# Kernel optimization log

Hardware: AMD Instinct MI355X
Metric: run time of the kernel (lower is better)

Reference implementation:

```python
import jax, jax.numpy as jnp
import numpy as np

N_WORDS = 8192   # total words across all concepts
L = 24           # chars per word (padded)
D = 256          # word_vec_d
H = 8            # attention heads
DFF = 1024
VOCAB = 128
N_CONCEPTS = 1024
MAXW = 16        # max_words
GROUPS = 4       # n_names: 4 equal groups of concepts


def setup_inputs() -> dict:
    key = jax.random.key(0)
    ks = jax.random.split(key, 9)
    rng = np.random.default_rng(0)
    # char tokens in [1, VOCAB), ragged word lengths in [4, L], tail = 0 (pad)
    vals = rng.integers(1, VOCAB, size=(N_WORDS, L))
    lens = rng.integers(4, L + 1, size=(N_WORDS,))
    inputs = np.where(np.arange(L)[None, :] < lens[:, None], vals, 0)
    # ragged words-per-concept: alternate 4 / 12 -> sums to N_WORDS, <= MAXW
    counts = np.where(np.arange(N_CONCEPTS) % 2 == 0, 4, 12)
    concept_id = np.repeat(np.arange(N_CONCEPTS), counts)
    word_pos = np.concatenate([np.arange(c) for c in counts])

    def w(k, shape):
        return 0.02 * jax.random.normal(k, shape, jnp.float32)

    return {
        "inputs": jnp.asarray(inputs, jnp.int32),
        "concept_id": jnp.asarray(concept_id, jnp.int32),
        "word_pos": jnp.asarray(word_pos, jnp.int32),
        "n_concepts": N_CONCEPTS,
        "n_names": GROUPS,
        "we_emb": w(ks[0], (VOCAB, D)),
        "we_qkv": w(ks[1], (D, 3 * D)),
        "we_o": w(ks[2], (D, D)),
        "we_ff1": w(ks[3], (D, DFF)),
        "we_ff2": w(ks[4], (DFF, D)),
        "ne_qkv": w(ks[5], (D, 3 * D)),
        "ne_o": w(ks[6], (D, D)),
        "ne_ff1": w(ks[7], (D, DFF)),
        "ne_ff2": w(ks[8], (DFF, D)),
    }


def _ln(x):
    m = x.mean(-1, keepdims=True)
    v = ((x - m) ** 2).mean(-1, keepdims=True)
    return (x - m) * jax.lax.rsqrt(v + 1e-5)


def _mha(x, wqkv, wo, key_pad=None):
    n, l, d = x.shape
    hd = d // H
    q, k, v = jnp.split(x @ wqkv, 3, axis=-1)
    q = q.reshape(n, l, H, hd)
    k = k.reshape(n, l, H, hd)
    v = v.reshape(n, l, H, hd)
    s = jnp.einsum('nqhd,nkhd->nhqk', q, k) / jnp.sqrt(jnp.asarray(hd, x.dtype))
    if key_pad is not None:
        s = jnp.where(key_pad[:, None, None, :], -1e9, s)
    a = jax.nn.softmax(s, axis=-1)
    o = jnp.einsum('nhqk,nkhd->nqhd', a, v).reshape(n, l, d)
    return o @ wo


def _block(x, wqkv, wo, w1, w2, key_pad=None):
    h = _ln(x + _mha(x, wqkv, wo, key_pad))
    return _ln(h + jax.nn.relu(h @ w1) @ w2)


def reference(inputs, concept_id, word_pos, n_concepts, n_names,
              we_emb, we_qkv, we_o, we_ff1, we_ff2,
              ne_qkv, ne_o, ne_ff1, ne_ff2):
    pad_mask = inputs == 0  # [N_WORDS, L]
    x = we_emb[inputs]      # [N_WORDS, L, D]
    word_ft = _block(x, we_qkv, we_o, we_ff1, we_ff2, pad_mask)
    # masked mean over chars -> one vector per word
    np_mask = (~pad_mask)[..., None].astype(word_ft.dtype)  # [N_WORDS, L, 1]
    name_vec = (word_ft * np_mask).sum(1) / np_mask.sum(1)   # [N_WORDS, D]
    # ragged -> padded: one scatter instead of per-sample torch.cat
    padded = jnp.zeros((n_concepts, MAXW, name_vec.shape[-1]), name_vec.dtype)
    padded = padded.at[concept_id, word_pos].set(name_vec)   # [n_concepts, MAXW, D]
    name_ft = _block(padded, ne_qkv, ne_o, ne_ff1, ne_ff2)
    row_pad = (padded == 0).all(-1, keepdims=True)           # all-zero rows = pad words
    name_ft = jnp.where(row_pad, jnp.zeros((), name_ft.dtype), name_ft)
    counts = (name_ft != 0).sum(1).astype(name_ft.dtype)     # [n_concepts, D]
    pooled = name_ft.sum(1) / counts                         # [n_concepts, D]
    return tuple(jnp.split(pooled, n_names, axis=0))
```

## Files before the change

kernel.cpp:

```cpp
#include <hip/hip_runtime.h>
#include <hip/hip_bf16.h>

#define NWORDS 8192
#define LW 24
#define DIM 256
#define NHEAD 8
#define DFF 1024
#define NCONC 1024
#define MAXW 16
#define TN (NCONC * MAXW)

typedef float floatx4 __attribute__((ext_vector_type(4)));
typedef short shortx8 __attribute__((ext_vector_type(8)));

__device__ __forceinline__ float bf2f(ushort u) {
  union { uint u; float f; } v; v.u = ((uint)u) << 16; return v.f;
}
__device__ __forceinline__ ushort f2bf(float f) {
  __hip_bfloat16 h = __float2bfloat16(f);
  return *reinterpret_cast<ushort*>(&h);
}

__device__ __forceinline__ void load_lds16(const ushort* gsrc, ushort* lds) {
  __builtin_amdgcn_global_load_lds((const __attribute__((address_space(1))) void*)gsrc,
                                   (__attribute__((address_space(3))) void*)lds, 16, 0, 0);
}

#define WAIT_VM0() __builtin_amdgcn_s_waitcnt(0x0F70)
#define WAIT_LGKM0() __builtin_amdgcn_s_waitcnt(0xC07F)

#define STAGE_COL(lane) ((((lane) & 3) ^ (((lane) >> 3) & 3)) * 8)
#define FRAG_OFF(row, quad) (((row) * 32) + ((((quad) ^ (((row) >> 1) & 3))) * 8))

struct WPSeg { const float* W; ushort* WT; int K; int N; int b0; };
struct WPAll { WPSeg seg[8]; };

__global__ __launch_bounds__(256) void wprep_all(WPAll a, int nseg) {
  int b = blockIdx.x;
  int s = 0;
#pragma unroll
  for (int i = 1; i < 8; i++)
    if (i < nseg && b >= a.seg[i].b0) s = i;
  const WPSeg sg = a.seg[s];
  int idx = (b - sg.b0) * 256 + threadIdx.x;
  if (idx < sg.K * sg.N) {
    int k = idx / sg.N, n = idx % sg.N;
    sg.WT[n * sg.K + k] = f2bf(sg.W[idx]);
  }
}

__global__ __launch_bounds__(256) void embed8(const int* __restrict__ inputs,
                                              const float* __restrict__ we_emb,
                                              ushort* __restrict__ x, int ntok) {
  int idx = blockIdx.x * 256 + threadIdx.x;
  int t = idx >> 5, d = (idx & 31) * 8;
  if (t < ntok) {
    const float4* src = (const float4*)&we_emb[inputs[t] * DIM + d];
    const float4 f0 = src[0], f1 = src[1];
    uint4 o;
    o.x = (uint)f2bf(f0.x) | ((uint)f2bf(f0.y) << 16);
    o.y = (uint)f2bf(f0.z) | ((uint)f2bf(f0.w) << 16);
    o.z = (uint)f2bf(f1.x) | ((uint)f2bf(f1.y) << 16);
    o.w = (uint)f2bf(f1.z) | ((uint)f2bf(f1.w) << 16);
    *(uint4*)&x[(size_t)t * DIM + d] = o;
  }
}

template <bool LN, int NTILES>
__global__ __launch_bounds__(256, 2) void gemm_tok64(const ushort* __restrict__ A, int lda,
                                                     const ushort* __restrict__ BT,
                                                     const ushort* __restrict__ RES,
                                                     ushort* __restrict__ C, int ldc) {
  __shared__ __align__(16) ushort As[8 * 64 * 32];
  __shared__ __align__(16) ushort Wb[256 * 32];
  __shared__ float red1[64 * 4];
  __shared__ float red2[64 * 4];
  const int tid = threadIdx.x;
  const int w = tid >> 6, lane = tid & 63;
  const int quad = lane >> 4, l16 = lane & 15;
  const long m0 = (long)blockIdx.y * 64;
  const long nb0 = (long)blockIdx.x * NTILES * 256;
  const int srow = lane >> 2;
  const int scol = STAGE_COL(lane);
  const int wc = w * 64;

#pragma unroll
  for (int t = 0; t < 8; t++) {
    int p = 2 * w + t / 4, ii = t % 4;
    load_lds16(&A[(m0 + ii * 16 + srow) * lda + p * 32 + scol], &As[p * 2048 + (ii * 16) * 32]);
  }
#pragma unroll
  for (int ii = 0; ii < 4; ii++)
    load_lds16(&BT[(nb0 + wc + ii * 16 + srow) * 256 + scol], &Wb[(wc + ii * 16) * 32]);
  __syncthreads();

#pragma unroll 1
  for (int nt = 0; nt < NTILES; nt++) {
    const long nb = nb0 + (long)nt * 256;
    floatx4 acc[4][4] = {};
#pragma unroll 1
    for (int p = 0; p < 8; p++) {
      WAIT_VM0();
      shortx8 a[4], b[4];
#pragma unroll
      for (int j = 0; j < 4; j++)
        b[j] = *(const shortx8*)&Wb[FRAG_OFF(wc + j * 16 + l16, quad)];
      WAIT_LGKM0();
      if (p < 7) {
#pragma unroll
        for (int ii = 0; ii < 4; ii++)
          load_lds16(&BT[(nb + wc + ii * 16 + srow) * 256 + (p + 1) * 32 + scol],
                     &Wb[(wc + ii * 16) * 32]);
      } else if (nt < NTILES - 1) {
#pragma unroll
        for (int ii = 0; ii < 4; ii++)
          load_lds16(&BT[(nb + 256 + wc + ii * 16 + srow) * 256 + scol],
                     &Wb[(wc + ii * 16) * 32]);
      }
#pragma unroll
      for (int i = 0; i < 4; i++)
        a[i] = *(const shortx8*)&As[p * 2048 + FRAG_OFF(i * 16 + l16, quad)];
#pragma unroll
      for (int i = 0; i < 4; i++)
#pragma unroll
        for (int j = 0; j < 4; j++)
          acc[i][j] = __builtin_amdgcn_mfma_f32_16x16x32_bf16(a[i], b[j], acc[i][j], 0, 0, 0);
    }

    if (!LN) {
#pragma unroll
      for (int i = 0; i < 4; i++)
#pragma unroll
        for (int j = 0; j < 4; j++)
#pragma unroll
          for (int r = 0; r < 4; r++) {
            long m = m0 + i * 16 + quad * 4 + r;
            C[m * ldc + nb + wc + j * 16 + l16] = f2bf(acc[i][j][r]);
          }
    } else {
#pragma unroll
      for (int i = 0; i < 4; i++)
#pragma unroll
        for (int r = 0; r < 4; r++) {
          int row = i * 16 + quad * 4 + r;
          float s1 = 0.f, s2 = 0.f;
#pragma unroll
          for (int j = 0; j < 4; j++) {
            float v = acc[i][j][r] + bf2f(RES[(m0 + row) * 256 + wc + j * 16 + l16]);
            acc[i][j][r] = v;
            s1 += v;
            s2 += v * v;
          }
#pragma unroll
          for (int off = 1; off < 16; off <<= 1) {
            s1 += __shfl_xor(s1, off);
            s2 += __shfl_xor(s2, off);
          }
          if (l16 == 0) { red1[row * 4 + w] = s1; red2[row * 4 + w] = s2; }
        }
      __syncthreads();
#pragma unroll
      for (int i = 0; i < 4; i++)
#pragma unroll
        for (int r = 0; r < 4; r++) {
          int row = i * 16 + quad * 4 + r;
          float s1 = red1[row * 4] + red1[row * 4 + 1] + red1[row * 4 + 2] + red1[row * 4 + 3];
          float s2 = red2[row * 4] + red2[row * 4 + 1] + red2[row * 4 + 2] + red2[row * 4 + 3];
          float mean = s1 * (1.f / 256.f);
          float rstd = rsqrtf(s2 * (1.f / 256.f) - mean * mean + 1e-5f);
#pragma unroll
          for (int j = 0; j < 4; j++)
            C[(m0 + row) * 256 + wc + j * 16 + l16] = f2bf((acc[i][j][r] - mean) * rstd);
        }
    }
  }
}

__global__ __launch_bounds__(256, 2) void ffn_fused(const ushort* __restrict__ H,
                                                    const ushort* __restrict__ W1T,
                                                    const ushort* __restrict__ W2T,
                                                    ushort* __restrict__ C,
                                                    int M) {
  __shared__ __align__(16) ushort As[8 * 64 * 32];
  __shared__ __align__(16) ushort Ss[8 * 64 * 32];
  __shared__ __align__(16) ushort Wb[256 * 32];
  const int tid = threadIdx.x;
  const int w = tid >> 6, lane = tid & 63;
  const int quad = lane >> 4, l16 = lane & 15;
  const long m0 = (long)blockIdx.x * 64;
  const int srow = lane >> 2;
  const int scol = STAGE_COL(lane);

#pragma unroll
  for (int t = 0; t < 8; t++) {
    int p = 2 * w + t / 4, ii = t % 4;
    load_lds16(&H[(m0 + ii * 16 + srow) * 256 + p * 32 + scol], &As[(p * 2048) + (ii * 16) * 32]);
  }
#pragma unroll
  for (int ii = 0; ii < 4; ii++)
    load_lds16(&W1T[(long)(w * 64 + ii * 16 + srow) * 256 + scol], &Wb[(w * 64 + ii * 16) * 32]);
  __syncthreads();

  floatx4 acc2[4][4] = {};
  for (int m = 0; m < 4; m++) {
    floatx4 acc1[4][4] = {};
    if (m > 0) {
#pragma unroll
      for (int ii = 0; ii < 4; ii++)
        load_lds16(&W1T[(long)(m * 256 + w * 64 + ii * 16 + srow) * 256 + scol],
                   &Wb[(w * 64 + ii * 16) * 32]);
    }
#pragma unroll 1
    for (int p = 0; p < 8; p++) {
      WAIT_VM0();
      shortx8 a[4], b[4];
#pragma unroll
      for (int i = 0; i < 4; i++)
        a[i] = *(const shortx8*)&Wb[FRAG_OFF(w * 64 + i * 16 + l16, quad)];
      WAIT_LGKM0();
      if (p < 7) {
#pragma unroll
        for (int ii = 0; ii < 4; ii++)
          load_lds16(&W1T[(long)(m * 256 + w * 64 + ii * 16 + srow) * 256 + (p + 1) * 32 + scol],
                     &Wb[(w * 64 + ii * 16) * 32]);
      }
#pragma unroll
      for (int j = 0; j < 4; j++)
        b[j] = *(const shortx8*)&As[p * 2048 + FRAG_OFF(j * 16 + l16, quad)];
#pragma unroll
      for (int i = 0; i < 4; i++)
#pragma unroll
        for (int j = 0; j < 4; j++)
          acc1[i][j] = __builtin_amdgcn_mfma_f32_16x16x32_bf16(a[i], b[j], acc1[i][j], 0, 0, 0);
    }
    __syncthreads();
#pragma unroll
    for (int i = 0; i < 4; i++) {
      int fb = w * 64 + i * 16 + quad * 4;
      int pf = fb >> 5, c = (fb >> 3) & 3, off = fb & 7;
#pragma unroll
      for (int j = 0; j < 4; j++) {
        int tok = j * 16 + l16;
        ushort4 pk;
        pk.x = f2bf(fmaxf(acc1[i][j][0], 0.f));
        pk.y = f2bf(fmaxf(acc1[i][j][1], 0.f));
        pk.z = f2bf(fmaxf(acc1[i][j][2], 0.f));
        pk.w = f2bf(fmaxf(acc1[i][j][3], 0.f));
        *(ushort4*)&Ss[(pf * 64 + tok) * 32 + ((c ^ ((tok >> 1) & 3)) << 3) + off] = pk;
      }
    }
    __syncthreads();
#pragma unroll
    for (int jj = 0; jj < 4; jj++)
      load_lds16(&W2T[(long)(w * 64 + jj * 16 + srow) * 1024 + m * 256 + scol],
                 &Wb[(w * 64 + jj * 16) * 32]);
#pragma unroll 1
    for (int p = 0; p < 8; p++) {
      WAIT_VM0();
      shortx8 a[4], b[4];
#pragma unroll
      for (int j = 0; j < 4; j++)
        b[j] = *(const shortx8*)&Wb[FRAG_OFF(w * 64 + j * 16 + l16, quad)];
      WAIT_LGKM0();
      if (p < 7) {
#pragma unroll
        for (int jj = 0; jj < 4; jj++)
          load_lds16(&W2T[(long)(w * 64 + jj * 16 + srow) * 1024 + m * 256 + (p + 1) * 32 + scol],
                     &Wb[(w * 64 + jj * 16) * 32]);
      }
#pragma unroll
      for (int i = 0; i < 4; i++)
        a[i] = *(const shortx8*)&Ss[p * 2048 + FRAG_OFF(i * 16 + l16, quad)];
#pragma unroll
      for (int i = 0; i < 4; i++)
#pragma unroll
        for (int j = 0; j < 4; j++)
          acc2[i][j] = __builtin_amdgcn_mfma_f32_16x16x32_bf16(a[i], b[j], acc2[i][j], 0, 0, 0);
    }
  }
  __syncthreads();

  float* red1 = (float*)Ss;
  float* red2 = red1 + 256;
  const int wc = w * 64;
#pragma unroll
  for (int i = 0; i < 4; i++)
#pragma unroll
    for (int r = 0; r < 4; r++) {
      int row = i * 16 + quad * 4 + r;
      float s1 = 0.f, s2 = 0.f;
#pragma unroll
      for (int j = 0; j < 4; j++) {
        float v = acc2[i][j][r] + bf2f(H[(m0 + row) * 256 + wc + j * 16 + l16]);
        acc2[i][j][r] = v;
        s1 += v;
        s2 += v * v;
      }
#pragma unroll
      for (int off = 1; off < 16; off <<= 1) {
        s1 += __shfl_xor(s1, off);
        s2 += __shfl_xor(s2, off);
      }
      if (l16 == 0) { red1[row * 4 + w] = s1; red2[row * 4 + w] = s2; }
    }
  __syncthreads();
#pragma unroll
  for (int i = 0; i < 4; i++)
#pragma unroll
    for (int r = 0; r < 4; r++) {
      int row = i * 16 + quad * 4 + r;
      float s1 = red1[row * 4] + red1[row * 4 + 1] + red1[row * 4 + 2] + red1[row * 4 + 3];
      float s2 = red2[row * 4] + red2[row * 4 + 1] + red2[row * 4 + 2] + red2[row * 4 + 3];
      float mean = s1 * (1.f / 256.f);
      float rstd = rsqrtf(s2 * (1.f / 256.f) - mean * mean + 1e-5f);
      if (m0 + row < M) {
#pragma unroll
        for (int j = 0; j < 4; j++)
          C[(m0 + row) * 256 + wc + j * 16 + l16] = f2bf((acc2[i][j][r] - mean) * rstd);
      }
    }
}

template <int LSEQ, bool MASKED>
__global__ __launch_bounds__(256) void attn(const int* __restrict__ inputs,
                                            ushort* __restrict__ qkv) {
  __shared__ __align__(16) ushort Qs[32 * 256];
  __shared__ __align__(16) ushort Ks[32 * 256];
  __shared__ __align__(16) ushort Vt[256 * 32];
  __shared__ __align__(16) ushort Ps[4 * 32 * 32];
  __shared__ float pads[32];
  constexpr int MT = (LSEQ + 15) / 16;
  const int blk = blockIdx.x;
  const int tid = threadIdx.x;
  const int w = tid >> 6, lane = tid & 63;
  const int quad = lane >> 4, l16 = lane & 15;
  ushort* base = qkv + (size_t)blk * LSEQ * 768;
  const uint4* src = (const uint4*)base;
  const uint4 z4 = {0u, 0u, 0u, 0u};

  for (int i = tid; i < (32 - LSEQ) * 32 * 2; i += 256) {
    int arr = (i >= (32 - LSEQ) * 32);
    int rem = arr ? i - (32 - LSEQ) * 32 : i;
    int row = LSEQ + (rem >> 5), ch = rem & 31;
    *(uint4*)&((arr ? Ks : Qs)[row * 256 + ch * 8]) = z4;
  }
  for (int i = tid; i < 256 * (4 - LSEQ / 8); i += 256) {
    int row = i & 255, pc = LSEQ / 8 + (i >> 8);
    *(uint4*)&Vt[row * 32 + ((pc ^ ((row >> 3) & 3)) * 8)] = z4;
  }
  {
    ushort* pz = Ps + w * 1024;
    *(uint4*)&pz[lane * 16] = z4;
    *(uint4*)&pz[lane * 16 + 8] = z4;
  }
  if (tid < 32) {
    float pv = 1.f;
    if (tid < LSEQ) pv = MASKED ? ((inputs[blk * LSEQ + tid] == 0) ? 1.f : 0.f) : 0.f;
    pads[tid] = pv;
  }
  for (int i = tid; i < LSEQ * 96; i += 256) {
    int c = i / 96, part = i % 96;
    uint4 val = src[c * 96 + part];
    int sect = part >> 5, off = part & 31;
    if (sect == 0) {
      *(uint4*)&Qs[c * 256 + ((off ^ (c & 7)) * 8)] = val;
    } else if (sect == 1) {
      *(uint4*)&Ks[c * 256 + ((off ^ (c & 7)) * 8)] = val;
    } else {
      int d0 = (off & 31) * 8;
      const ushort* us = (const ushort*)&val;
#pragma unroll
      for (int j = 0; j < 8; j++) {
        int dim = d0 + j;
        Vt[dim * 32 + (((c >> 3) ^ ((dim >> 3) & 3)) * 8) + (c & 7)] = us[j];
      }
    }
  }
  __syncthreads();

  ushort* Psw = Ps + w * 1024;
#pragma unroll
  for (int t = 0; t < 2; t++) {
    const int h = w * 2 + t, hb = h * 32;
    shortx8 aq[MT], bk[MT];
#pragma unroll
    for (int i = 0; i < MT; i++)
      aq[i] = *(const shortx8*)&Qs[(i * 16 + l16) * 256 + (((h * 4 + quad) ^ (l16 & 7)) * 8)];
#pragma unroll
    for (int j = 0; j < MT; j++)
      bk[j] = *(const shortx8*)&Ks[(j * 16 + l16) * 256 + (((h * 4 + quad) ^ (l16 & 7)) * 8)];
    floatx4 s[MT][MT];
#pragma unroll
    for (int i = 0; i < MT; i++)
#pragma unroll
      for (int j = 0; j < MT; j++) {
        floatx4 zz = {0.f, 0.f, 0.f, 0.f};
        s[i][j] = __builtin_amdgcn_mfma_f32_16x16x32_bf16(aq[i], bk[j], zz, 0, 0, 0);
      }
    float pv[MT];
#pragma unroll
    for (int j = 0; j < MT; j++) pv[j] = pads[j * 16 + l16];
#pragma unroll
    for (int i = 0; i < MT; i++) {
#pragma unroll
      for (int r = 0; r < 4; r++) {
        float v[MT];
        float mx = -3e38f;
#pragma unroll
        for (int j = 0; j < MT; j++) {
          float x = s[i][j][r] * 0.17677669529663687f;
          if (pv[j] != 0.f) x = -1e9f;
          v[j] = x;
          mx = fmaxf(mx, x);
        }
#pragma unroll
        for (int off = 1; off < 16; off <<= 1) mx = fmaxf(mx, __shfl_xor(mx, off));
        float den = 0.f;
#pragma unroll
        for (int j = 0; j < MT; j++) { v[j] = __expf(v[j] - mx); den += v[j]; }
#pragma unroll
        for (int off = 1; off < 16; off <<= 1) den += __shfl_xor(den, off);
        float inv = 1.f / den;
        int row = i * 16 + quad * 4 + r;
#pragma unroll
        for (int j = 0; j < MT; j++) {
          int col = j * 16 + l16;
          Psw[row * 32 + (((col >> 3) ^ ((row >> 1) & 3)) * 8) + (col & 7)] = f2bf(v[j] * inv);
        }
      }
    }
    WAIT_LGKM0();
    shortx8 pa[MT], bv[2];
#pragma unroll
    for (int i = 0; i < MT; i++) {
      int row = i * 16 + l16;
      pa[i] = *(const shortx8*)&Psw[row * 32 + ((quad ^ ((row >> 1) & 3)) * 8)];
    }
#pragma unroll
    for (int jj = 0; jj < 2; jj++) {
      int row = hb + jj * 16 + l16;
      bv[jj] = *(const shortx8*)&Vt[row * 32 + ((quad ^ ((row >> 3) & 3)) * 8)];
    }
    floatx4 o[MT][2];
#pragma unroll
    for (int i = 0; i < MT; i++)
#pragma unroll
      for (int jj = 0; jj < 2; jj++) {
        floatx4 zz = {0.f, 0.f, 0.f, 0.f};
        o[i][jj] = __builtin_amdgcn_mfma_f32_16x16x32_bf16(pa[i], bv[jj], zz, 0, 0, 0);
      }
#pragma unroll
    for (int i = 0; i < MT; i++)
#pragma unroll
      for (int r = 0; r < 4; r++) {
        int row = i * 16 + quad * 4 + r;
        if (row < LSEQ) {
#pragma unroll
          for (int jj = 0; jj < 2; jj++)
            base[(size_t)row * 768 + hb + jj * 16 + l16] = f2bf(o[i][jj][r]);
        }
      }
  }
}

__global__ __launch_bounds__(256) void pool_scatter(const ushort* __restrict__ ft,
                                                    const int* __restrict__ inputs,
                                                    const int* __restrict__ cid,
                                                    const int* __restrict__ wpos,
                                                    ushort* __restrict__ padded,
                                                    int* __restrict__ flags) {
  int w = blockIdx.x, d = threadIdx.x;
  float s = 0.f;
  int cnt = 0;
  for (int c = 0; c < LW; c++) {
    if (inputs[w * LW + c] != 0) {
      s += bf2f(ft[((size_t)w * LW + c) * DIM + d]);
      cnt++;
    }
  }
  int slot = cid[w] * MAXW + wpos[w];
  padded[(size_t)slot * DIM + d] = f2bf(s / (float)cnt);
  if (d == 0) flags[slot] = 1;
}

__global__ __launch_bounds__(256) void final_pool(const ushort* __restrict__ nft,
                                                  const int* __restrict__ flags,
                                                  float* __restrict__ out) {
  int n = blockIdx.x, d = threadIdx.x;
  float s = 0.f;
  int cnt = 0;
  for (int wd = 0; wd < MAXW; wd++) {
    if (flags[n * MAXW + wd]) {
      s += bf2f(nft[((size_t)n * MAXW + wd) * DIM + d]);
      cnt++;
    }
  }
  out[n * DIM + d] = s / (float)cnt;
}

extern "C" void kernel_launch(void* const* d_in, const int* in_sizes, int n_in,
                              void* d_out, int out_size, void* d_ws, size_t ws_size,
                              hipStream_t stream) {
  const int* inputs = (const int*)d_in[0];
  const int* cid = (const int*)d_in[1];
  const int* wpos = (const int*)d_in[2];
  const float* we_emb = (const float*)d_in[5];
  const float* we_qkv = (const float*)d_in[6];
  const float* we_o = (const float*)d_in[7];
  const float* we_ff1 = (const float*)d_in[8];
  const float* we_ff2 = (const float*)d_in[9];
  const float* ne_qkv = (const float*)d_in[10];
  const float* ne_o = (const float*)d_in[11];
  const float* ne_ff1 = (const float*)d_in[12];
  const float* ne_ff2 = (const float*)d_in[13];
  float* out = (float*)d_out;

  int chunks = 4;
  if (ws_size >= 515000000UL) chunks = 1;
  else if (ws_size >= 263258112UL) chunks = 2;
  const int wpc = NWORDS / chunks;
  const int tpc = wpc * LW;

  const size_t X = (size_t)tpc * DIM * 2;
  const size_t Q = (size_t)tpc * 768 * 2;

  char* base = (char*)d_ws;
  ushort* x = (ushort*)(base);
  ushort* qkv = (ushort*)(base + X);
  ushort* h = (ushort*)(base + X + Q);
  ushort* ft = qkv;
  size_t pend = X + Q + X;
  ushort* padded = (ushort*)(base + pend);
  int* flags = (int*)(base + pend + 8388608);
  ushort* wT = (ushort*)(base + pend + 8454144);
  ushort* nqkv = (ushort*)(base);
  ushort* nh = (ushort*)(base + 25165824);
  ushort* nft = (ushort*)(base + 33554432);

  ushort* wqkvT = wT;
  ushort* woT = wT + 196608;
  ushort* wff1T = wT + 262144;
  ushort* wff2T = wT + 524288;
  ushort* nqkvT = wT + 786432;
  ushort* neoT = wT + 983040;
  ushort* neff1T = wT + 1048576;
  ushort* neff2T = wT + 1310720;

  {
    WPAll a;
    a.seg[0] = {we_qkv, wqkvT, 256, 768, 0};
    a.seg[1] = {we_o, woT, 256, 256, 768};
    a.seg[2] = {we_ff1, wff1T, 256, 1024, 1024};
    a.seg[3] = {we_ff2, wff2T, 1024, 256, 2048};
    a.seg[4] = {ne_qkv, nqkvT, 256, 768, 3072};
    a.seg[5] = {ne_o, neoT, 256, 256, 3840};
    a.seg[6] = {ne_ff1, neff1T, 256, 1024, 4096};
    a.seg[7] = {ne_ff2, neff2T, 1024, 256, 5120};
    wprep_all<<<6144, 256, 0, stream>>>(a, 8);
  }

  (void)hipMemsetAsync(padded, 0, (size_t)TN * DIM * 2, stream);
  (void)hipMemsetAsync(flags, 0, TN * 4, stream);

  for (int c = 0; c < chunks; c++) {
    const int* in_c = inputs + (size_t)c * wpc * LW;
    const int* cid_c = cid + (size_t)c * wpc;
    const int* wpos_c = wpos + (size_t)c * wpc;

    embed8<<<tpc / 8, 256, 0, stream>>>(in_c, we_emb, x, tpc);
    {
      dim3 g(1, tpc / 64);
      gemm_tok64<false, 3><<<g, 256, 0, stream>>>(x, 256, wqkvT, nullptr, qkv, 768);
    }
    attn<24, true><<<wpc, 256, 0, stream>>>(in_c, qkv);
    {
      dim3 g(1, tpc / 64);
      gemm_tok64<true, 1><<<g, 256, 0, stream>>>(qkv, 768, woT, x, h, 256);
    }
    ffn_fused<<<tpc / 64, 256, 0, stream>>>(h, wff1T, wff2T, ft, tpc);
    pool_scatter<<<wpc, 256, 0, stream>>>(ft, in_c, cid_c, wpos_c, padded, flags);
  }

  {
    dim3 g(1, TN / 64);
    gemm_tok64<false, 3><<<g, 256, 0, stream>>>(padded, 256, nqkvT, nullptr, nqkv, 768);
  }
  attn<16, false><<<NCONC, 256, 0, stream>>>(nullptr, nqkv);
  {
    dim3 g(1, TN / 64);
    gemm_tok64<true, 1><<<g, 256, 0, stream>>>(nqkv, 768, neoT, padded, nh, 256);
  }
  ffn_fused<<<TN / 64, 256, 0, stream>>>(nh, neff1T, neff2T, nft, TN);
  final_pool<<<NCONC, 256, 0, stream>>>(nft, flags, out);
}
```

Measured before the change: 888.8 us.

## Fuse word-level QKV projection with attention in a single kernel

Adds a kernel that computes the QKV projection for two words (48 tokens) per block, keeps Q, K and transposed V in swizzled shared memory, and runs masked softmax attention there with MFMA. Only the attention output goes to global memory. This removes the round trip of the 768-wide QKV tensor through HBM and one kernel launch. In exchange the block uses a large amount of LDS at one block per SM, and its 48-row tiles leave some MFMA work on padded rows, so occupancy and tile efficiency may drop.

```diff
diff --git a/kernel.cpp b/kernel.cpp
--- a/kernel.cpp
+++ b/kernel.cpp
@@ -176,6 +176,187 @@
   }
 }
 
+__global__ __launch_bounds__(256, 1) void qkv_attn_fused(
+    const ushort* __restrict__ A,
+    const ushort* __restrict__ BT,
+    const int* __restrict__ inputs,
+    ushort* __restrict__ O) {
+  constexpr int LSEQ = 24, WPB = 2, ROWS = WPB * LSEQ;
+  __shared__ __align__(16) ushort As[8 * ROWS * 32];
+  __shared__ __align__(16) ushort Wb[256 * 32];
+  __shared__ __align__(16) ushort Qs[WPB][24 * 256];
+  __shared__ __align__(16) ushort Ks[WPB][24 * 256];
+  __shared__ __align__(16) ushort Vt[WPB][256 * 32];
+  __shared__ __align__(16) ushort Ps[4][32 * 32];
+  __shared__ float pads[WPB][32];
+  const int tid = threadIdx.x;
+  const int w = tid >> 6, lane = tid & 63;
+  const int quad = lane >> 4, l16 = lane & 15;
+  const int blk = blockIdx.x;
+  const long m0 = (long)blk * ROWS;
+  const int srow = lane >> 2;
+  const int scol = STAGE_COL(lane);
+  const int wc = w * 64;
+
+  if (tid < WPB * 32) {
+    int wd = tid >> 5, r = tid & 31;
+    pads[wd][r] = (r >= LSEQ || inputs[(blk * WPB + wd) * LW + r] == 0) ? 1.f : 0.f;
+  }
+#pragma unroll
+  for (int t = 0; t < 6; t++) {
+    int idx = w * 6 + t, p = idx / 3, ii = idx % 3;
+    load_lds16(&A[(m0 + ii * 16 + srow) * 256 + p * 32 + scol],
+               &As[p * (ROWS * 32) + (ii * 16) * 32]);
+  }
+#pragma unroll
+  for (int ii = 0; ii < 4; ii++)
+    load_lds16(&BT[(wc + ii * 16 + srow) * 256 + scol], &Wb[(wc + ii * 16) * 32]);
+  __syncthreads();
+
+#pragma unroll 1
+  for (int nt = 0; nt < 3; nt++) {
+    const long nb = (long)nt * 256;
+    floatx4 acc[3][4] = {};
+#pragma unroll 1
+    for (int p = 0; p < 8; p++) {
+      WAIT_VM0();
+      shortx8 a[3], b[4];
+#pragma unroll
+      for (int j = 0; j < 4; j++)
+        b[j] = *(const shortx8*)&Wb[FRAG_OFF(wc + j * 16 + l16, quad)];
+      WAIT_LGKM0();
+      if (p < 7) {
+#pragma unroll
+        for (int ii = 0; ii < 4; ii++)
+          load_lds16(&BT[(nb + wc + ii * 16 + srow) * 256 + (p + 1) * 32 + scol],
+                     &Wb[(wc + ii * 16) * 32]);
+      } else if (nt < 2) {
+#pragma unroll
+        for (int ii = 0; ii < 4; ii++)
+          load_lds16(&BT[(nb + 256 + wc + ii * 16 + srow) * 256 + scol],
+                     &Wb[(wc + ii * 16) * 32]);
+      }
+#pragma unroll
+      for (int i = 0; i < 3; i++)
+        a[i] = *(const shortx8*)&As[p * (ROWS * 32) + FRAG_OFF(i * 16 + l16, quad)];
+#pragma unroll
+      for (int i = 0; i < 3; i++)
+#pragma unroll
+        for (int j = 0; j < 4; j++)
+          acc[i][j] = __builtin_amdgcn_mfma_f32_16x16x32_bf16(a[i], b[j], acc[i][j], 0, 0, 0);
+    }
+#pragma unroll
+    for (int i = 0; i < 3; i++)
+#pragma unroll
+      for (int r = 0; r < 4; r++) {
+        int row = i * 16 + quad * 4 + r;
+        int wd = (row >= LSEQ) ? 1 : 0;
+        int tok = row - wd * LSEQ;
+#pragma unroll
+        for (int j = 0; j < 4; j++) {
+          int dim = wc + j * 16 + l16;
+          ushort val = f2bf(acc[i][j][r]);
+          if (nt == 0) {
+            Qs[wd][tok * 256 + (((dim >> 3) ^ (tok & 7)) << 3) + (dim & 7)] = val;
+          } else if (nt == 1) {
+            Ks[wd][tok * 256 + (((dim >> 3) ^ (tok & 7)) << 3) + (dim & 7)] = val;
+          } else {
+            Vt[wd][dim * 32 + ((((tok >> 3) ^ ((dim >> 3) & 3))) << 3) + (tok & 7)] = val;
+          }
+        }
+      }
+  }
+  __syncthreads();
+
+  const int wd = w >> 1;
+  ushort* Psw = Ps[w];
+  const ushort* Qw = Qs[wd];
+  const ushort* Kw = Ks[wd];
+  const ushort* Vw = Vt[wd];
+#pragma unroll 1
+  for (int t = 0; t < 4; t++) {
+    const int h = (w & 1) * 4 + t, hb = h * 32;
+    shortx8 aq[2], bk[2];
+#pragma unroll
+    for (int i = 0; i < 2; i++)
+      aq[i] = *(const shortx8*)&Qw[(i * 16 + l16) * 256 + (((h * 4 + quad) ^ (l16 & 7)) * 8)];
+#pragma unroll
+    for (int j = 0; j < 2; j++)
+      bk[j] = *(const shortx8*)&Kw[(j * 16 + l16) * 256 + (((h * 4 + quad) ^ (l16 & 7)) * 8)];
+    floatx4 s[2][2];
+#pragma unroll
+    for (int i = 0; i < 2; i++)
+#pragma unroll
+      for (int j = 0; j < 2; j++) {
+        floatx4 zz = {0.f, 0.f, 0.f, 0.f};
+        s[i][j] = __builtin_amdgcn_mfma_f32_16x16x32_bf16(aq[i], bk[j], zz, 0, 0, 0);
+      }
+    float pv[2];
+#pragma unroll
+    for (int j = 0; j < 2; j++) pv[j] = pads[wd][j * 16 + l16];
+#pragma unroll
+    for (int i = 0; i < 2; i++) {
+#pragma unroll
+      for (int r = 0; r < 4; r++) {
+        float v[2];
+        float mx = -3e38f;
+#pragma unroll
+        for (int j = 0; j < 2; j++) {
+          float x = s[i][j][r] * 0.17677669529663687f;
+          if (pv[j] != 0.f) x = -1e9f;
+          v[j] = x;
+          mx = fmaxf(mx, x);
+        }
+#pragma unroll
+        for (int off = 1; off < 16; off <<= 1) mx = fmaxf(mx, __shfl_xor(mx, off));
+        float den = 0.f;
+#pragma unroll
+        for (int j = 0; j < 2; j++) { v[j] = __expf(v[j] - mx); den += v[j]; }
+#pragma unroll
+        for (int off = 1; off < 16; off <<= 1) den += __shfl_xor(den, off);
+        float inv = 1.f / den;
+        int row = i * 16 + quad * 4 + r;
+#pragma unroll
+        for (int j = 0; j < 2; j++) {
+          int col = j * 16 + l16;
+          Psw[row * 32 + (((col >> 3) ^ ((row >> 1) & 3)) * 8) + (col & 7)] = f2bf(v[j] * inv);
+        }
+      }
+    }
+    WAIT_LGKM0();
+    shortx8 pa[2], bv[2];
+#pragma unroll
+    for (int i = 0; i < 2; i++) {
+      int row = i * 16 + l16;
+      pa[i] = *(const shortx8*)&Psw[row * 32 + ((quad ^ ((row >> 1) & 3)) * 8)];
+    }
+#pragma unroll
+    for (int jj = 0; jj < 2; jj++) {
+      int row = hb + jj * 16 + l16;
+      bv[jj] = *(const shortx8*)&Vw[row * 32 + ((quad ^ ((row >> 3) & 3)) * 8)];
+    }
+    floatx4 o[2][2];
+#pragma unroll
+    for (int i = 0; i < 2; i++)
+#pragma unroll
+      for (int jj = 0; jj < 2; jj++) {
+        floatx4 zz = {0.f, 0.f, 0.f, 0.f};
+        o[i][jj] = __builtin_amdgcn_mfma_f32_16x16x32_bf16(pa[i], bv[jj], zz, 0, 0, 0);
+      }
+#pragma unroll
+    for (int i = 0; i < 2; i++)
+#pragma unroll
+      for (int r = 0; r < 4; r++) {
+        int row = i * 16 + quad * 4 + r;
+        if (row < LSEQ) {
+#pragma unroll
+          for (int jj = 0; jj < 2; jj++)
+            O[(m0 + wd * LSEQ + row) * 256 + hb + jj * 16 + l16] = f2bf(o[i][jj][r]);
+        }
+      }
+  }
+}
+
 __global__ __launch_bounds__(256, 2) void ffn_fused(const ushort* __restrict__ H,
                                                     const ushort* __restrict__ W1T,
                                                     const ushort* __restrict__ W2T,
@@ -526,9 +707,9 @@
 
   char* base = (char*)d_ws;
   ushort* x = (ushort*)(base);
-  ushort* qkv = (ushort*)(base + X);
+  ushort* obuf = (ushort*)(base + X);
   ushort* h = (ushort*)(base + X + Q);
-  ushort* ft = qkv;
+  ushort* ft = obuf;
   size_t pend = X + Q + X;
   ushort* padded = (ushort*)(base + pend);
   int* flags = (int*)(base + pend + 8388608);
@@ -568,14 +749,10 @@
     const int* wpos_c = wpos + (size_t)c * wpc;
 
     embed8<<<tpc / 8, 256, 0, stream>>>(in_c, we_emb, x, tpc);
+    qkv_attn_fused<<<tpc / 48, 256, 0, stream>>>(x, wqkvT, in_c, obuf);
     {
       dim3 g(1, tpc / 64);
-      gemm_tok64<false, 3><<<g, 256, 0, stream>>>(x, 256, wqkvT, nullptr, qkv, 768);
-    }
-    attn<24, true><<<wpc, 256, 0, stream>>>(in_c, qkv);
-    {
-      dim3 g(1, tpc / 64);
-      gemm_tok64<true, 1><<<g, 256, 0, stream>>>(qkv, 768, woT, x, h, 256);
+      gemm_tok64<true, 1><<<g, 256, 0, stream>>>(obuf, 256, woT, x, h, 256);
     }
     ffn_fused<<<tpc / 64, 256, 0, stream>>>(h, wff1T, wff2T, ft, tpc);
     pool_scatter<<<wpc, 256, 0, stream>>>(ft, in_c, cid_c, wpos_c, padded, flags);
```

Result: slower. 978.1 us (+10.0%).

## Fuse attention output projection and LayerNorm into the FFN kernel

Applied to the files above, without the earlier changes.

Merges the separate Wo projection GEMM (with residual add and LayerNorm) into the FFN kernel. Each 64-token block computes the projection from the attention output, normalizes it into shared memory, and runs the FFN on it directly. This removes one kernel launch per stage and the write and re-read of the intermediate h buffer, and the FFN residual now comes from LDS. In exchange the fused kernel does more serial work per block and uses more registers, which may lower occupancy.

```diff
diff --git a/kernel.cpp b/kernel.cpp
--- a/kernel.cpp
+++ b/kernel.cpp
@@ -176,11 +176,14 @@
   }
 }
 
-__global__ __launch_bounds__(256, 2) void ffn_fused(const ushort* __restrict__ H,
-                                                    const ushort* __restrict__ W1T,
-                                                    const ushort* __restrict__ W2T,
-                                                    ushort* __restrict__ C,
-                                                    int M) {
+__global__ __launch_bounds__(256, 2) void oproj_ffn_fused(
+    const ushort* __restrict__ QKV,
+    const ushort* __restrict__ XR,
+    const ushort* __restrict__ WoT,
+    const ushort* __restrict__ W1T,
+    const ushort* __restrict__ W2T,
+    ushort* __restrict__ C,
+    int M) {
   __shared__ __align__(16) ushort As[8 * 64 * 32];
   __shared__ __align__(16) ushort Ss[8 * 64 * 32];
   __shared__ __align__(16) ushort Wb[256 * 32];
@@ -190,15 +193,89 @@
   const long m0 = (long)blockIdx.x * 64;
   const int srow = lane >> 2;
   const int scol = STAGE_COL(lane);
+  const int wc = w * 64;
 
 #pragma unroll
   for (int t = 0; t < 8; t++) {
     int p = 2 * w + t / 4, ii = t % 4;
-    load_lds16(&H[(m0 + ii * 16 + srow) * 256 + p * 32 + scol], &As[(p * 2048) + (ii * 16) * 32]);
+    load_lds16(&QKV[(m0 + ii * 16 + srow) * 768 + p * 32 + scol], &Ss[p * 2048 + (ii * 16) * 32]);
   }
 #pragma unroll
   for (int ii = 0; ii < 4; ii++)
-    load_lds16(&W1T[(long)(w * 64 + ii * 16 + srow) * 256 + scol], &Wb[(w * 64 + ii * 16) * 32]);
+    load_lds16(&WoT[(long)(wc + ii * 16 + srow) * 256 + scol], &Wb[(wc + ii * 16) * 32]);
+  __syncthreads();
+
+  floatx4 aco[4][4] = {};
+#pragma unroll 1
+  for (int p = 0; p < 8; p++) {
+    WAIT_VM0();
+    shortx8 a[4], b[4];
+#pragma unroll
+    for (int j = 0; j < 4; j++)
+      b[j] = *(const shortx8*)&Wb[FRAG_OFF(wc + j * 16 + l16, quad)];
+    WAIT_LGKM0();
+    if (p < 7) {
+#pragma unroll
+      for (int ii = 0; ii < 4; ii++)
+        load_lds16(&WoT[(long)(wc + ii * 16 + srow) * 256 + (p + 1) * 32 + scol],
+                   &Wb[(wc + ii * 16) * 32]);
+    }
+#pragma unroll
+    for (int i = 0; i < 4; i++)
+      a[i] = *(const shortx8*)&Ss[p * 2048 + FRAG_OFF(i * 16 + l16, quad)];
+#pragma unroll
+    for (int i = 0; i < 4; i++)
+#pragma unroll
+      for (int j = 0; j < 4; j++)
+        aco[i][j] = __builtin_amdgcn_mfma_f32_16x16x32_bf16(a[i], b[j], aco[i][j], 0, 0, 0);
+  }
+  __syncthreads();
+
+  {
+    float* red1 = (float*)Ss;
+    float* red2 = red1 + 256;
+#pragma unroll
+    for (int i = 0; i < 4; i++)
+#pragma unroll
+      for (int r = 0; r < 4; r++) {
+        int row = i * 16 + quad * 4 + r;
+        float s1 = 0.f, s2 = 0.f;
+#pragma unroll
+        for (int j = 0; j < 4; j++) {
+          float v = aco[i][j][r] + bf2f(XR[(m0 + row) * 256 + wc + j * 16 + l16]);
+          aco[i][j][r] = v;
+          s1 += v;
+          s2 += v * v;
+        }
+#pragma unroll
+        for (int off = 1; off < 16; off <<= 1) {
+          s1 += __shfl_xor(s1, off);
+          s2 += __shfl_xor(s2, off);
+        }
+        if (l16 == 0) { red1[row * 4 + w] = s1; red2[row * 4 + w] = s2; }
+      }
+    __syncthreads();
+#pragma unroll
+    for (int i = 0; i < 4; i++)
+#pragma unroll
+      for (int r = 0; r < 4; r++) {
+        int row = i * 16 + quad * 4 + r;
+        float s1 = red1[row * 4] + red1[row * 4 + 1] + red1[row * 4 + 2] + red1[row * 4 + 3];
+        float s2 = red2[row * 4] + red2[row * 4 + 1] + red2[row * 4 + 2] + red2[row * 4 + 3];
+        float mean = s1 * (1.f / 256.f);
+        float rstd = rsqrtf(s2 * (1.f / 256.f) - mean * mean + 1e-5f);
+#pragma unroll
+        for (int j = 0; j < 4; j++) {
+          int col = wc + j * 16 + l16;
+          int p = col >> 5, c = (col >> 3) & 3, off = col & 7;
+          As[p * 2048 + row * 32 + ((c ^ ((row >> 1) & 3)) << 3) + off] =
+              f2bf((aco[i][j][r] - mean) * rstd);
+        }
+      }
+  }
+#pragma unroll
+  for (int ii = 0; ii < 4; ii++)
+    load_lds16(&W1T[(long)(wc + ii * 16 + srow) * 256 + scol], &Wb[(wc + ii * 16) * 32]);
   __syncthreads();
 
   floatx4 acc2[4][4] = {};
@@ -207,8 +284,8 @@
     if (m > 0) {
 #pragma unroll
       for (int ii = 0; ii < 4; ii++)
-        load_lds16(&W1T[(long)(m * 256 + w * 64 + ii * 16 + srow) * 256 + scol],
-                   &Wb[(w * 64 + ii * 16) * 32]);
+        load_lds16(&W1T[(long)(m * 256 + wc + ii * 16 + srow) * 256 + scol],
+                   &Wb[(wc + ii * 16) * 32]);
     }
 #pragma unroll 1
     for (int p = 0; p < 8; p++) {
@@ -216,13 +293,13 @@
       shortx8 a[4], b[4];
 #pragma unroll
       for (int i = 0; i < 4; i++)
-        a[i] = *(const shortx8*)&Wb[FRAG_OFF(w * 64 + i * 16 + l16, quad)];
+        a[i] = *(const shortx8*)&Wb[FRAG_OFF(wc + i * 16 + l16, quad)];
       WAIT_LGKM0();
       if (p < 7) {
 #pragma unroll
         for (int ii = 0; ii < 4; ii++)
-          load_lds16(&W1T[(long)(m * 256 + w * 64 + ii * 16 + srow) * 256 + (p + 1) * 32 + scol],
-                     &Wb[(w * 64 + ii * 16) * 32]);
+          load_lds16(&W1T[(long)(m * 256 + wc + ii * 16 + srow) * 256 + (p + 1) * 32 + scol],
+                     &Wb[(wc + ii * 16) * 32]);
       }
 #pragma unroll
       for (int j = 0; j < 4; j++)
@@ -236,7 +313,7 @@
     __syncthreads();
 #pragma unroll
     for (int i = 0; i < 4; i++) {
-      int fb = w * 64 + i * 16 + quad * 4;
+      int fb = wc + i * 16 + quad * 4;
       int pf = fb >> 5, c = (fb >> 3) & 3, off = fb & 7;
 #pragma unroll
       for (int j = 0; j < 4; j++) {
@@ -252,21 +329,21 @@
     __syncthreads();
 #pragma unroll
     for (int jj = 0; jj < 4; jj++)
-      load_lds16(&W2T[(long)(w * 64 + jj * 16 + srow) * 1024 + m * 256 + scol],
-                 &Wb[(w * 64 + jj * 16) * 32]);
+      load_lds16(&W2T[(long)(wc + jj * 16 + srow) * 1024 + m * 256 + scol],
+                 &Wb[(wc + jj * 16) * 32]);
 #pragma unroll 1
     for (int p = 0; p < 8; p++) {
       WAIT_VM0();
       shortx8 a[4], b[4];
 #pragma unroll
       for (int j = 0; j < 4; j++)
-        b[j] = *(const shortx8*)&Wb[FRAG_OFF(w * 64 + j * 16 + l16, quad)];
+        b[j] = *(const shortx8*)&Wb[FRAG_OFF(wc + j * 16 + l16, quad)];
       WAIT_LGKM0();
       if (p < 7) {
 #pragma unroll
         for (int jj = 0; jj < 4; jj++)
-          load_lds16(&W2T[(long)(w * 64 + jj * 16 + srow) * 1024 + m * 256 + (p + 1) * 32 + scol],
-                     &Wb[(w * 64 + jj * 16) * 32]);
+          load_lds16(&W2T[(long)(wc + jj * 16 + srow) * 1024 + m * 256 + (p + 1) * 32 + scol],
+                     &Wb[(wc + jj * 16) * 32]);
       }
 #pragma unroll
       for (int i = 0; i < 4; i++)
@@ -282,7 +359,6 @@
 
   float* red1 = (float*)Ss;
   float* red2 = red1 + 256;
-  const int wc = w * 64;
 #pragma unroll
   for (int i = 0; i < 4; i++)
 #pragma unroll
@@ -291,7 +367,10 @@
       float s1 = 0.f, s2 = 0.f;
 #pragma unroll
       for (int j = 0; j < 4; j++) {
-        float v = acc2[i][j][r] + bf2f(H[(m0 + row) * 256 + wc + j * 16 + l16]);
+        int col = wc + j * 16 + l16;
+        int p = col >> 5, c = (col >> 3) & 3, off = col & 7;
+        float hval = bf2f(As[p * 2048 + row * 32 + ((c ^ ((row >> 1) & 3)) << 3) + off]);
+        float v = acc2[i][j][r] + hval;
         acc2[i][j][r] = v;
         s1 += v;
         s2 += v * v;
@@ -527,14 +606,12 @@
   char* base = (char*)d_ws;
   ushort* x = (ushort*)(base);
   ushort* qkv = (ushort*)(base + X);
-  ushort* h = (ushort*)(base + X + Q);
-  ushort* ft = qkv;
+  ushort* ft = (ushort*)(base + X + Q);
   size_t pend = X + Q + X;
   ushort* padded = (ushort*)(base + pend);
   int* flags = (int*)(base + pend + 8388608);
   ushort* wT = (ushort*)(base + pend + 8454144);
   ushort* nqkv = (ushort*)(base);
-  ushort* nh = (ushort*)(base + 25165824);
   ushort* nft = (ushort*)(base + 33554432);
 
   ushort* wqkvT = wT;
@@ -573,11 +650,7 @@
       gemm_tok64<false, 3><<<g, 256, 0, stream>>>(x, 256, wqkvT, nullptr, qkv, 768);
     }
     attn<24, true><<<wpc, 256, 0, stream>>>(in_c, qkv);
-    {
-      dim3 g(1, tpc / 64);
-      gemm_tok64<true, 1><<<g, 256, 0, stream>>>(qkv, 768, woT, x, h, 256);
-    }
-    ffn_fused<<<tpc / 64, 256, 0, stream>>>(h, wff1T, wff2T, ft, tpc);
+    oproj_ffn_fused<<<tpc / 64, 256, 0, stream>>>(qkv, x, woT, wff1T, wff2T, ft, tpc);
     pool_scatter<<<wpc, 256, 0, stream>>>(ft, in_c, cid_c, wpos_c, padded, flags);
   }
 
@@ -586,10 +659,6 @@
     gemm_tok64<false, 3><<<g, 256, 0, stream>>>(padded, 256, nqkvT, nullptr, nqkv, 768);
   }
   attn<16, false><<<NCONC, 256, 0, stream>>>(nullptr, nqkv);
-  {
-    dim3 g(1, TN / 64);
-    gemm_tok64<true, 1><<<g, 256, 0, stream>>>(nqkv, 768, neoT, padded, nh, 256);
-  }
-  ffn_fused<<<TN / 64, 256, 0, stream>>>(nh, neff1T, neff2T, nft, TN);
+  oproj_ffn_fused<<<TN / 64, 256, 0, stream>>>(nqkv, padded, neoT, neff1T, neff2T, nft, TN);
   final_pool<<<NCONC, 256, 0, stream>>>(nft, flags, out);
 }
```

Measured after the change: 1.058 ms. 19.0% more time.
